# Performance work log

Measured on AMD Instinct MI355X. Metric: run time of the kernel, lower is better.

The kernel has to match this reference:

```python
import jax, jax.numpy as jnp
import numpy as np

TWO_PI = 2.0 * np.pi


def _fftfreq(n, d):
    # numpy-compatible fftfreq, trace/grad-safe in d: [0..n/2-1, -n/2..-1]/(n*d)
    k = jnp.arange(n)
    k = jnp.where(k < (n + 1) // 2, k, k - n).astype(jnp.float32)
    return k / (n * d)


def _forward(x, wp1_re, wp1_im, wp2_re, wp2_im, wr_re, wr_im, ty, tx):
    wp1 = (wp1_re + 1j * wp1_im).astype(jnp.complex64)   # [Ci,Co,m1]
    wp2 = (wp2_re + 1j * wp2_im).astype(jnp.complex64)   # [Ci,Co,m2]
    wr = (wr_re + 1j * wr_im).astype(jnp.complex64)      # [Ci,Co,m1,m2]
    Ny, Nx = x.shape[-2], x.shape[-1]
    dty = ty[1] - ty[0]
    dtx = tx[1] - tx[0]

    alpha = jnp.fft.fft2(x, axes=(-2, -1))               # [B,Ci,Ny,Nx] complex
    lam1 = (1j * TWO_PI * _fftfreq(Ny, dty)).astype(jnp.complex64)  # [Ny]
    lam2 = (1j * TWO_PI * _fftfreq(Nx, dtx)).astype(jnp.complex64)  # [Nx]

    # Pole-residue transfer function factors: Hw = wr / ((lam1-p1)(lam2-p2))
    A1 = 1.0 / (lam1 - wp1[..., None])                   # [Ci,Co,m1,Ny]
    A2 = 1.0 / (lam2 - wp2[..., None])                   # [Ci,Co,m2,Nx]

    # sum over poles (p,q) of Hw -> [Ci,Co,Ny,Nx]
    Hsum = jnp.einsum('ikpq,ikpo,ikqx->ikox', wr, A1, A2)
    res1 = jnp.einsum('biox,ikox->bkox', alpha, Hsum)    # [B,Co,Ny,Nx]
    # sum over frequency grid (o,x) -> residue coefficients [B,Co,m1,m2]
    res2 = jnp.einsum('biox,ikpq,ikpo,ikqx->bkpq', alpha, wr, A1, A2)

    x1 = jnp.real(jnp.fft.ifft2(res1, s=(Ny, Nx), axes=(-2, -1)))

    # explicit pole-exponential evaluation over the spatial grid
    E1 = jnp.exp(wp1[..., None] * ty.astype(jnp.complex64))  # [Ci,Co,m1,Ny]
    E2 = jnp.exp(wp2[..., None] * tx.astype(jnp.complex64))  # [Ci,Co,m2,Nx]
    # res2 channel dim contracts against E1/E2's first (in==out required)
    x2 = jnp.real(jnp.einsum('kbpq,bipz,biqx->kizx', res2, E1, E2)) / (Nx * Ny)
    return x1 + x2


def setup_inputs() -> dict:
    key = jax.random.key(0)
    B, Ci, Co, Ny, Nx, m1, m2 = 8, 32, 32, 128, 128, 4, 5
    ks = jax.random.split(key, 7)
    scale = 1.0 / (Ci * Co)
    x = jax.random.normal(ks[0], (B, Ci, Ny, Nx), jnp.float32)
    wp1_re = scale * jax.random.uniform(ks[1], (Ci, Co, m1), jnp.float32)
    wp1_im = scale * jax.random.uniform(ks[2], (Ci, Co, m1), jnp.float32)
    wp2_re = scale * jax.random.uniform(ks[3], (Ci, Co, m2), jnp.float32)
    wp2_im = scale * jax.random.uniform(ks[4], (Ci, Co, m2), jnp.float32)
    wr_re = scale * jax.random.uniform(ks[5], (Ci, Co, m1, m2), jnp.float32)
    wr_im = scale * jax.random.uniform(ks[6], (Ci, Co, m1, m2), jnp.float32)
    ty = (jnp.arange(Ny) / Ny).astype(jnp.float32)
    tx = (jnp.arange(Nx) / Nx).astype(jnp.float32)
    return dict(x=x, wp1_re=wp1_re, wp1_im=wp1_im, wp2_re=wp2_re, wp2_im=wp2_im,
                wr_re=wr_re, wr_im=wr_im, ty=ty, tx=tx)


def reference(x, wp1_re, wp1_im, wp2_re, wp2_im, wr_re, wr_im, ty, tx):
    return _forward(x, wp1_re, wp1_im, wp2_re, wp2_im, wr_re, wr_im, ty, tx)
```

## Files before the change

kernel.cpp:

```cpp
#include <hip/hip_runtime.h>
#include <math.h>

#define N 128
#define B 8
#define CI 32
#define CO 32
#define M1 4
#define M2 5
#define IK (CI*CO)
#define IKP (IK*M1)
#define IKQ (IK*M2)
#define TWO_PI_F 6.2831853071795864769f

__device__ __forceinline__ float2 cmul(float2 a, float2 b){
    return make_float2(fmaf(a.x,b.x,-(a.y*b.y)), fmaf(a.x,b.y,a.y*b.x));
}
__device__ __forceinline__ float2 cmadd(float2 acc, float2 a, float2 b){
    acc.x = fmaf(a.x, b.x, fmaf(-a.y, b.y, acc.x));
    acc.y = fmaf(a.x, b.y, fmaf( a.y, b.x, acc.y));
    return acc;
}

__global__ void k_A1T(const float* wr_, const float* wi_, const float* t_, float2* A1T){
    int idx = blockIdx.x*256 + threadIdx.x;
    int o   = idx >> 12;
    int ikp = idx & (IKP-1);
    float d = t_[1]-t_[0];
    float invnd = 1.0f/((float)N*d);
    int kk = (o < N/2) ? o : o - N;
    float lam = TWO_PI_F * (float)kk * invnd;
    float dr = -wr_[ikp];
    float di = lam - wi_[ikp];
    float inv = 1.0f/(dr*dr + di*di);
    A1T[idx] = make_float2(dr*inv, -di*inv);
}

__global__ void k_A2(const float* wr_, const float* wi_, const float* t_, float2* A2){
    int idx = blockIdx.x*256 + threadIdx.x;
    int ikq = idx >> 7; int xx = idx & (N-1);
    float d = t_[1]-t_[0];
    float invnd = 1.0f/((float)N*d);
    int kk = (xx < N/2) ? xx : xx - N;
    float lam = TWO_PI_F * (float)kk * invnd;
    float dr = -wr_[ikq];
    float di = lam - wi_[ikq];
    float inv = 1.0f/(dr*dr + di*di);
    A2[idx] = make_float2(dr*inv, -di*inv);
}

__global__ void k_E(const float* wr_, const float* wi_, const float* t_, float2* E){
    int idx = blockIdx.x*256 + threadIdx.x;
    int ikp = idx >> 7; int y = idx & (N-1);
    float t = t_[y];
    float m = expf(wr_[ikp]*t);
    float s, c; sincosf(wi_[ikp]*t, &s, &c);
    E[idx] = make_float2(m*c, m*s);
}

__global__ void k_W2N(const float* wrr, const float* wri, const float2* A2, float2* W2N){
    int idx = blockIdx.x*256 + threadIdx.x;
    int ikp = idx >> 7; int xx = idx & (N-1);
    int ik = ikp >> 2; int p = ikp & 3;
    float2 acc = make_float2(0.f,0.f);
    const float* wr0 = wrr + ik*(M1*M2) + p*M2;
    const float* wi0 = wri + ik*(M1*M2) + p*M2;
    const float2* a2 = A2 + (size_t)ik*(M2*N) + xx;
    #pragma unroll
    for(int q=0;q<M2;q++){
        float2 w = make_float2(wr0[q], wi0[q]);
        acc = cmadd(acc, w, a2[q*N]);
    }
    W2N[(size_t)ikp*N + xx] = acc;
}

template<int SIGNPOS, int REALIN, int SCALE>
__global__ void __launch_bounds__(256) k_fft_rows(const void* in_, float2* out){
    const float sgn = SIGNPOS ? 1.0f : -1.0f;
    __shared__ float tre[16*132];
    __shared__ float tim_[16*132];
    __shared__ float zre[16*136];
    __shared__ float zim[16*136];
    int t = threadIdx.x;
    size_t row0 = (size_t)blockIdx.x * 16;

    if(REALIN){
        const float* src = (const float*)in_ + row0*N;
        #pragma unroll
        for(int j=0;j<8;j++){
            int idx = t + 256*j; int r = idx>>7, cl = idx&127;
            tre[r*132+cl] = src[idx];
        }
    } else {
        const float2* src = (const float2*)in_ + row0*N;
        #pragma unroll
        for(int j=0;j<8;j++){
            int idx = t + 256*j; int r = idx>>7, cl = idx&127;
            float2 v = src[idx];
            tre[r*132+cl] = v.x; tim_[r*132+cl] = v.y;
        }
    }
    float t16c[16], t16s[16];
    #pragma unroll
    for(int j=0;j<16;j++){ float s,c; sincosf(sgn*(TWO_PI_F/16.f)*(float)j, &s,&c); t16c[j]=c; t16s[j]=s; }
    __syncthreads();

    int r = t>>4, u = t&15, b = u&7, h = u>>3;
    float xr[16], xi[16];
    #pragma unroll
    for(int a=0;a<16;a++){
        float vr = tre[r*132 + 8*a + b];
        float vi = REALIN ? 0.f : tim_[r*132 + 8*a + b];
        if(h && (a&1)){ vr = -vr; vi = -vi; }
        xr[a]=vr; xi[a]=vi;
    }
    #pragma unroll
    for(int cc=0; cc<8; cc++){
        float yr=0.f, yi=0.f;
        #pragma unroll
        for(int a=0;a<16;a++){
            int j = (a*cc)&15;
            if(REALIN){
                yr = fmaf(xr[a], t16c[j], yr);
                yi = fmaf(xr[a], t16s[j], yi);
            } else {
                yr = fmaf(xr[a], t16c[j], yr); yr = fmaf(-xi[a], t16s[j], yr);
                yi = fmaf(xr[a], t16s[j], yi); yi = fmaf( xi[a], t16c[j], yi);
            }
        }
        int c = 8*h + cc;
        float s,co; sincosf(sgn*(TWO_PI_F/128.f)*(float)(b*c), &s,&co);
        zre[r*136 + b*17 + c] = fmaf(yr,co,-(yi*s));
        zim[r*136 + b*17 + c] = fmaf(yr,s,  yi*co);
    }
    __syncthreads();

    float t8c[8], t8s[8];
    #pragma unroll
    for(int j=0;j<8;j++){ float s,c; sincosf(sgn*(TWO_PI_F/8.f)*(float)j, &s,&c); t8c[j]=c; t8s[j]=s; }
    int r2 = t>>4, c2 = t&15;
    float zr_[8], zi_[8];
    #pragma unroll
    for(int bb=0;bb<8;bb++){ zr_[bb]=zre[r2*136 + bb*17 + c2]; zi_[bb]=zim[r2*136 + bb*17 + c2]; }
    float2* dst = out + (row0 + r2)*N;
    #pragma unroll
    for(int d=0; d<8; d++){
        float Xr=0.f, Xi=0.f;
        #pragma unroll
        for(int bb=0;bb<8;bb++){
            int j=(bb*d)&7;
            Xr = fmaf(zr_[bb], t8c[j], Xr); Xr = fmaf(-zi_[bb], t8s[j], Xr);
            Xi = fmaf(zr_[bb], t8s[j], Xi); Xi = fmaf( zi_[bb], t8c[j], Xi);
        }
        if(SCALE){ Xr *= (1.f/128.f); Xi *= (1.f/128.f); }
        dst[c2 + 16*d] = make_float2(Xr, Xi);
    }
}

template<int SIGNPOS, int REALOUT, int SCALE>
__global__ void __launch_bounds__(256) k_fft_cols(const float2* in, float2* outc, float* outr){
    const float sgn = SIGNPOS ? 1.0f : -1.0f;
    __shared__ float tre[N*17];
    __shared__ float tim_[N*17];
    __shared__ float zre[8*16*17];
    __shared__ float zim[8*16*17];
    int t = threadIdx.x;
    int img = blockIdx.x >> 3; int x0 = (blockIdx.x & 7)*16;
    const float2* src = in + (size_t)img*N*N + x0;
    #pragma unroll
    for(int j=0;j<8;j++){
        int idx = t + 256*j; int y = idx>>4, xc = idx&15;
        float2 v = src[y*N + xc];
        tre[y*17+xc]=v.x; tim_[y*17+xc]=v.y;
    }
    float t16c[16], t16s[16];
    #pragma unroll
    for(int j=0;j<16;j++){ float s,c; sincosf(sgn*(TWO_PI_F/16.f)*(float)j, &s,&c); t16c[j]=c; t16s[j]=s; }
    __syncthreads();

    int xc = t&15, u = t>>4, b = u&7, h = u>>3;
    float xr[16], xi[16];
    #pragma unroll
    for(int a=0;a<16;a++){
        int y = 8*a + b;
        float vr = tre[y*17+xc];
        float vi = tim_[y*17+xc];
        if(h && (a&1)){ vr = -vr; vi = -vi; }
        xr[a]=vr; xi[a]=vi;
    }
    #pragma unroll
    for(int cc=0; cc<8; cc++){
        float yr=0.f, yi=0.f;
        #pragma unroll
        for(int a=0;a<16;a++){
            int j = (a*cc)&15;
            yr = fmaf(xr[a], t16c[j], yr); yr = fmaf(-xi[a], t16s[j], yr);
            yi = fmaf(xr[a], t16s[j], yi); yi = fmaf( xi[a], t16c[j], yi);
        }
        int c = 8*h + cc;
        float s,co; sincosf(sgn*(TWO_PI_F/128.f)*(float)(b*c), &s,&co);
        zre[(b*16 + c)*17 + xc] = fmaf(yr,co,-(yi*s));
        zim[(b*16 + c)*17 + xc] = fmaf(yr,s,  yi*co);
    }
    __syncthreads();

    float t8c[8], t8s[8];
    #pragma unroll
    for(int j=0;j<8;j++){ float s,c; sincosf(sgn*(TWO_PI_F/8.f)*(float)j, &s,&c); t8c[j]=c; t8s[j]=s; }
    int c2 = t>>4; int x2 = t&15;
    float zr_[8], zi_[8];
    #pragma unroll
    for(int bb=0;bb<8;bb++){ zr_[bb]=zre[(bb*16 + c2)*17 + x2]; zi_[bb]=zim[(bb*16 + c2)*17 + x2]; }
    #pragma unroll
    for(int d=0; d<8; d++){
        float Xr=0.f, Xi=0.f;
        #pragma unroll
        for(int bb=0;bb<8;bb++){
            int j=(bb*d)&7;
            Xr = fmaf(zr_[bb], t8c[j], Xr); Xr = fmaf(-zi_[bb], t8s[j], Xr);
            Xi = fmaf(zr_[bb], t8s[j], Xi); Xi = fmaf( zi_[bb], t8c[j], Xi);
        }
        int ky = c2 + 16*d;
        if(REALOUT){
            outr[(size_t)img*N*N + ky*N + x0 + x2] = Xr * (SCALE ? (1.f/128.f) : 1.f);
        } else {
            if(SCALE){ Xr *= (1.f/128.f); Xi *= (1.f/128.f); }
            outc[(size_t)img*N*N + ky*N + x0 + x2] = make_float2(Xr, Xi);
        }
    }
}

__global__ void __launch_bounds__(256) k_res1(const float2* alpha, const float2* A1T,
                                              const float2* W2N, float2* res1){
    __shared__ float4 At4[B*CI*8];
    int t = threadIdx.x;
    int o  = blockIdx.x >> 3;
    int x0 = (blockIdx.x & 7) * 16;

    {
        int im0 = t >> 3, xq = t & 7;
        #pragma unroll
        for(int j=0;j<8;j++){
            int im = im0 + 32*j;
            At4[im*8 + xq] = *(const float4*)(alpha + (size_t)im*(N*N) + o*N + x0 + 2*xq);
        }
    }
    __syncthreads();

    int k = t >> 3, xh = t & 7;
    float2 acc[B][2];
    #pragma unroll
    for(int b=0;b<B;b++){ acc[b][0]=make_float2(0.f,0.f); acc[b][1]=make_float2(0.f,0.f); }

    const float2* a1base = A1T + (size_t)o*IKP + k*M1;
    const float2* w2base = W2N + ((size_t)k*M1)*N + x0 + 2*xh;

    #pragma unroll 2
    for(int i=0;i<CI;i++){
        float4 a1a = *(const float4*)(a1base + (size_t)i*128);
        float4 a1b = *(const float4*)(a1base + (size_t)i*128 + 2);
        float2 a1v[M1] = { make_float2(a1a.x,a1a.y), make_float2(a1a.z,a1a.w),
                           make_float2(a1b.x,a1b.y), make_float2(a1b.z,a1b.w) };
        float2 h0 = make_float2(0.f,0.f), h1 = make_float2(0.f,0.f);
        const float2* w2 = w2base + (size_t)i*(128*N);
        #pragma unroll
        for(int p=0;p<M1;p++){
            float4 wv = *(const float4*)(w2 + (size_t)p*N);
            h0 = cmadd(h0, a1v[p], make_float2(wv.x,wv.y));
            h1 = cmadd(h1, a1v[p], make_float2(wv.z,wv.w));
        }
        #pragma unroll
        for(int b=0;b<B;b++){
            float4 av = At4[(b*CI + i)*8 + xh];
            acc[b][0] = cmadd(acc[b][0], make_float2(av.x,av.y), h0);
            acc[b][1] = cmadd(acc[b][1], make_float2(av.z,av.w), h1);
        }
    }

    #pragma unroll
    for(int b=0;b<B;b++){
        float4 v = make_float4(acc[b][0].x, acc[b][0].y, acc[b][1].x, acc[b][1].y);
        *(float4*)(res1 + (size_t)(b*CO + k)*(N*N) + o*N + x0 + 2*xh) = v;
    }
}

__global__ void __launch_bounds__(256) k_S_res2(const float2* alpha, const float2* A2,
                                                const float2* A1T, const float* wrr,
                                                const float* wri, float2* res2){
    __shared__ float2 tile[128*17];
    __shared__ float2 A2c[16*40];
    int t = threadIdx.x;
    int ol = t & 31;
    int kl = t >> 5;
    int bid = blockIdx.x;
    int kq = bid & 3;
    int i  = (bid >> 2) & (CI-1);
    int b  = bid >> 7;
    int k0 = kq*8;
    int k  = k0 + kl;
    int ik = i*CO + k;
    const float2* asrc = alpha + ((size_t)(b*CI + i))*(N*N);

    const int trow = t >> 4, txc = t & 15;
    int a2dst[3]; size_t a2src[3]; bool a2ok[3];
    #pragma unroll
    for(int s=0;s<3;s++){
        int e = t + 256*s;
        a2ok[s] = (e < 640);
        int e2 = a2ok[s] ? e : 0;
        int xcs = e2 / 40, rs = e2 - xcs*40;
        int kk = rs / 5, qq = rs - kk*5;
        a2dst[s] = xcs*40 + rs;
        a2src[s] = ((size_t)(i*CO + k0 + kk)*M2 + qq)*N + xcs;
    }

    float2 U[4][5];
    #pragma unroll
    for(int oi=0;oi<4;oi++)
        #pragma unroll
        for(int q=0;q<5;q++) U[oi][q] = make_float2(0.f,0.f);

    float2 pre[8], a2pre[3];
    #pragma unroll
    for(int j=0;j<8;j++) pre[j] = asrc[(trow + 16*j)*N + txc];
    #pragma unroll
    for(int s=0;s<3;s++) if(a2ok[s]) a2pre[s] = A2[a2src[s]];

    for(int c=0; c<8; c++){
        __syncthreads();
        #pragma unroll
        for(int j=0;j<8;j++) tile[(trow + 16*j)*17 + txc] = pre[j];
        #pragma unroll
        for(int s=0;s<3;s++) if(a2ok[s]) A2c[a2dst[s]] = a2pre[s];
        if(c < 7){
            int x0n = (c+1)*16;
            #pragma unroll
            for(int j=0;j<8;j++) pre[j] = asrc[(trow + 16*j)*N + x0n + txc];
            #pragma unroll
            for(int s=0;s<3;s++) if(a2ok[s]) a2pre[s] = A2[a2src[s] + x0n];
        }
        __syncthreads();
        #pragma unroll 4
        for(int xc=0; xc<16; xc++){
            float2 a2v[5];
            const float2* a2row = A2c + xc*40 + kl*5;
            #pragma unroll
            for(int q=0;q<5;q++) a2v[q] = a2row[q];
            #pragma unroll
            for(int oi=0;oi<4;oi++){
                float2 av = tile[(ol + 32*oi)*17 + xc];
                #pragma unroll
                for(int q=0;q<5;q++) U[oi][q] = cmadd(U[oi][q], av, a2v[q]);
            }
        }
    }

    float2 S[4][5];
    #pragma unroll
    for(int p=0;p<4;p++)
        #pragma unroll
        for(int q=0;q<5;q++) S[p][q] = make_float2(0.f,0.f);
    #pragma unroll
    for(int oi=0;oi<4;oi++){
        int o = ol + 32*oi;
        const float2* a1 = A1T + (size_t)o*IKP + (size_t)ik*M1;
        float2 a1v[4];
        #pragma unroll
        for(int p=0;p<4;p++) a1v[p] = a1[p];
        #pragma unroll
        for(int p=0;p<4;p++)
            #pragma unroll
            for(int q=0;q<5;q++) S[p][q] = cmadd(S[p][q], a1v[p], U[oi][q]);
    }
    #pragma unroll
    for(int m=1;m<32;m<<=1){
        #pragma unroll
        for(int p=0;p<4;p++)
            #pragma unroll
            for(int q=0;q<5;q++){
                S[p][q].x += __shfl_xor(S[p][q].x, m);
                S[p][q].y += __shfl_xor(S[p][q].y, m);
            }
    }
    if(ol==0){
        const float* wr0 = wrr + ik*(M1*M2);
        const float* wi0 = wri + ik*(M1*M2);
        float2* dst = res2 + (size_t)(b*CO + k)*(M1*M2);
        #pragma unroll
        for(int p=0;p<4;p++)
            #pragma unroll
            for(int q=0;q<5;q++){
                float2 w = make_float2(wr0[p*5+q], wi0[p*5+q]);
                float2 v = cmul(w, S[p][q]);
                atomicAdd(&dst[p*5+q].x, v.x);
                atomicAdd(&dst[p*5+q].y, v.y);
            }
    }
}

__global__ void __launch_bounds__(256) k_x2(const float2* res2, const float2* E1,
                                            const float2* E2, float* out){
    __shared__ __align__(16) float2 res2s[CI*M1*M2];
    __shared__ __align__(16) float2 Wt[M1*N];
    __shared__ __align__(16) float2 buf[2][M1*64 + M2*N];
    int t = threadIdx.x;
    int yh = blockIdx.x & 1;
    int j  = (blockIdx.x >> 1) & (CO-1);
    int b  = blockIdx.x >> 6;
    int xt = t & 15, yt = t >> 4;

    {
        const float4* s4 = (const float4*)(res2 + (size_t)b*CO*M1*M2);
        float4* d4 = (float4*)res2s;
        d4[t] = s4[t];
        if(t < 64) d4[256+t] = s4[256+t];
    }

    const bool is1_0 = (t < 128);
    const bool ok1 = (t < 192);
    int off0, dst0;
    if(is1_0){ int pp = t >> 5, rem = t & 31; off0 = pp*N + rem*2; dst0 = pp*64 + rem*2; }
    else     { int g = t - 128; int qq = g >> 6, xi = (g & 63) << 1; off0 = qq*N + xi; dst0 = 256 + qq*128 + xi; }
    int qq1 = 2 + (t >> 6), xi1 = (t & 63) << 1;
    int off1 = qq1*N + xi1;
    int dst1 = 256 + qq1*128 + xi1;

    const float2* E1c = E1 + ((size_t)j*M1)*N + yh*64;
    const float2* E2c = E2 + ((size_t)j*M2)*N;

    float4 pre0 = *(const float4*)((is1_0 ? E1c : E2c) + off0);
    float4 pre1 = ok1 ? *(const float4*)(E2c + off1) : make_float4(0.f,0.f,0.f,0.f);
    *(float4*)(&buf[0][dst0]) = pre0;
    if(ok1) *(float4*)(&buf[0][dst1]) = pre1;
    int cur = 0;
    __syncthreads();

    float acc[4][8];
    #pragma unroll
    for(int yy=0;yy<4;yy++)
        #pragma unroll
        for(int s=0;s<8;s++) acc[yy][s] = 0.f;

    for(int c=0; c<CI; c++){
        const float2* E2s = buf[cur] + 256;
        #pragma unroll
        for(int s=0;s<2;s++){
            int e = t + 256*s;
            int pp = e >> 7, xi = e & 127;
            const float2* rr = res2s + c*(M1*M2) + pp*M2;
            float2 w = make_float2(0.f,0.f);
            #pragma unroll
            for(int q=0;q<M2;q++) w = cmadd(w, rr[q], E2s[q*128 + xi]);
            Wt[pp*128 + xi] = w;
        }
        if(c+1 < CI){
            E1c += (size_t)CO*M1*N;
            E2c += (size_t)CO*M2*N;
            pre0 = *(const float4*)((is1_0 ? E1c : E2c) + off0);
            if(ok1) pre1 = *(const float4*)(E2c + off1);
        }
        __syncthreads();

        const float2* E1s = buf[cur];
        float2 e1[4][4];
        #pragma unroll
        for(int p=0;p<4;p++){
            float4 a  = *(const float4*)(E1s + p*64 + yt*4);
            float4 bq = *(const float4*)(E1s + p*64 + yt*4 + 2);
            e1[p][0]=make_float2(a.x,a.y);  e1[p][1]=make_float2(a.z,a.w);
            e1[p][2]=make_float2(bq.x,bq.y); e1[p][3]=make_float2(bq.z,bq.w);
        }
        #pragma unroll
        for(int p=0;p<4;p++){
            #pragma unroll
            for(int s=0;s<4;s++){
                float4 wv = *(const float4*)(Wt + p*128 + 32*s + 2*xt);
                #pragma unroll
                for(int yy=0;yy<4;yy++){
                    float2 e = e1[p][yy];
                    acc[yy][2*s]   = fmaf(e.x, wv.x, fmaf(-e.y, wv.y, acc[yy][2*s]));
                    acc[yy][2*s+1] = fmaf(e.x, wv.z, fmaf(-e.y, wv.w, acc[yy][2*s+1]));
                }
            }
        }
        if(c+1 < CI){
            float2* nb = buf[cur^1];
            *(float4*)(nb + dst0) = pre0;
            if(ok1) *(float4*)(nb + dst1) = pre1;
        }
        cur ^= 1;
        __syncthreads();
    }

    const float sc = 1.0f/((float)N*(float)N);
    size_t base = (size_t)(b*CO + j)*(N*N) + (size_t)yh*64*N;
    #pragma unroll
    for(int yy=0;yy<4;yy++){
        float* orow = out + base + (size_t)(yt*4 + yy)*N;
        #pragma unroll
        for(int s=0;s<4;s++){
            float2* dst = (float2*)(orow + 32*s + 2*xt);
            float2 old = *dst;
            *dst = make_float2(old.x + acc[yy][2*s]*sc, old.y + acc[yy][2*s+1]*sc);
        }
    }
}

extern "C" void kernel_launch(void* const* d_in, const int* in_sizes, int n_in,
                              void* d_out, int out_size, void* d_ws, size_t ws_size,
                              hipStream_t stream){
    const float* x    = (const float*)d_in[0];
    const float* wp1r = (const float*)d_in[1];
    const float* wp1i = (const float*)d_in[2];
    const float* wp2r = (const float*)d_in[3];
    const float* wp2i = (const float*)d_in[4];
    const float* wrr  = (const float*)d_in[5];
    const float* wri  = (const float*)d_in[6];
    const float* ty   = (const float*)d_in[7];
    const float* tx   = (const float*)d_in[8];
    float* out = (float*)d_out;
    float2* ws = (float2*)d_ws;

    const size_t NCIMG = (size_t)B*CI*N*N;
    float2* bufA  = ws;
    float2* alpha = bufA  + NCIMG;
    float2* res1  = alpha + NCIMG;
    float2* A1T   = res1  + NCIMG;
    float2* A2    = A1T   + (size_t)N*IKP;
    float2* W2N   = A2    + (size_t)IKQ*N;
    float2* E1    = W2N   + (size_t)N*IKP;
    float2* E2    = E1    + (size_t)IKP*N;
    float2* res2  = E2    + (size_t)IKQ*N;

    k_A1T<<<(N*IKP)/256, 256, 0, stream>>>(wp1r, wp1i, ty, A1T);
    k_E  <<<(IKP*N)/256, 256, 0, stream>>>(wp1r, wp1i, ty, E1);
    k_A2 <<<(IKQ*N)/256, 256, 0, stream>>>(wp2r, wp2i, tx, A2);
    k_E  <<<(IKQ*N)/256, 256, 0, stream>>>(wp2r, wp2i, tx, E2);
    k_W2N<<<(IKP*N)/256, 256, 0, stream>>>(wrr, wri, A2, W2N);

    k_fft_rows<0,1,0><<<(B*CI*N)/16, 256, 0, stream>>>((const void*)x, bufA);
    k_fft_cols<0,0,0><<<B*CI*8, 256, 0, stream>>>(bufA, alpha, nullptr);

    hipMemsetAsync(res2, 0, (size_t)B*CO*M1*M2*sizeof(float2), stream);
    k_res1<<<N*8, 256, 0, stream>>>(alpha, A1T, W2N, res1);
    k_S_res2<<<B*CI*4, 256, 0, stream>>>(alpha, A2, A1T, wrr, wri, res2);

    k_fft_rows<1,0,1><<<(B*CO*N)/16, 256, 0, stream>>>((const void*)res1, bufA);
    k_fft_cols<1,1,1><<<B*CO*8, 256, 0, stream>>>(bufA, nullptr, out);
    k_x2<<<B*CO*2, 256, 0, stream>>>(res2, E1, E2, out);
}
```

Baseline: 355.2 us.

## Enlarge per-block work tiles in res2 and x2 kernels to reuse loads

```diff
diff --git a/kernel.cpp b/kernel.cpp
--- a/kernel.cpp
+++ b/kernel.cpp
@@ -287,67 +287,65 @@
                                                 const float2* A1T, const float* wrr,
                                                 const float* wri, float2* res2){
     __shared__ float2 tile[128*17];
-    __shared__ float2 A2c[16*40];
+    __shared__ float2 A2c[16*80];
     int t = threadIdx.x;
-    int ol = t & 31;
-    int kl = t >> 5;
+    int ol = t & 15;
+    int kl = t >> 4;
     int bid = blockIdx.x;
-    int kq = bid & 3;
-    int i  = (bid >> 2) & (CI-1);
-    int b  = bid >> 7;
-    int k0 = kq*8;
+    int kh = bid & 1;
+    int i  = (bid >> 1) & (CI-1);
+    int b  = bid >> 6;
+    int k0 = kh*16;
     int k  = k0 + kl;
     int ik = i*CO + k;
     const float2* asrc = alpha + ((size_t)(b*CI + i))*(N*N);
 
     const int trow = t >> 4, txc = t & 15;
-    int a2dst[3]; size_t a2src[3]; bool a2ok[3];
-    #pragma unroll
-    for(int s=0;s<3;s++){
+    int a2dst[5]; size_t a2src[5];
+    #pragma unroll
+    for(int s=0;s<5;s++){
         int e = t + 256*s;
-        a2ok[s] = (e < 640);
-        int e2 = a2ok[s] ? e : 0;
-        int xcs = e2 / 40, rs = e2 - xcs*40;
+        int xcs = e / 80, rs = e - xcs*80;
         int kk = rs / 5, qq = rs - kk*5;
-        a2dst[s] = xcs*40 + rs;
+        a2dst[s] = xcs*80 + rs;
         a2src[s] = ((size_t)(i*CO + k0 + kk)*M2 + qq)*N + xcs;
     }
 
-    float2 U[4][5];
-    #pragma unroll
-    for(int oi=0;oi<4;oi++)
+    float2 U[8][5];
+    #pragma unroll
+    for(int oi=0;oi<8;oi++)
         #pragma unroll
         for(int q=0;q<5;q++) U[oi][q] = make_float2(0.f,0.f);
 
-    float2 pre[8], a2pre[3];
+    float2 pre[8], a2pre[5];
     #pragma unroll
     for(int j=0;j<8;j++) pre[j] = asrc[(trow + 16*j)*N + txc];
     #pragma unroll
-    for(int s=0;s<3;s++) if(a2ok[s]) a2pre[s] = A2[a2src[s]];
+    for(int s=0;s<5;s++) a2pre[s] = A2[a2src[s]];
 
     for(int c=0; c<8; c++){
         __syncthreads();
         #pragma unroll
         for(int j=0;j<8;j++) tile[(trow + 16*j)*17 + txc] = pre[j];
         #pragma unroll
-        for(int s=0;s<3;s++) if(a2ok[s]) A2c[a2dst[s]] = a2pre[s];
+        for(int s=0;s<5;s++) A2c[a2dst[s]] = a2pre[s];
         if(c < 7){
             int x0n = (c+1)*16;
             #pragma unroll
             for(int j=0;j<8;j++) pre[j] = asrc[(trow + 16*j)*N + x0n + txc];
             #pragma unroll
-            for(int s=0;s<3;s++) if(a2ok[s]) a2pre[s] = A2[a2src[s] + x0n];
+            for(int s=0;s<5;s++) a2pre[s] = A2[a2src[s] + x0n];
         }
         __syncthreads();
-        #pragma unroll 4
+        #pragma unroll 2
         for(int xc=0; xc<16; xc++){
             float2 a2v[5];
-            const float2* a2row = A2c + xc*40 + kl*5;
+            const float2* a2row = A2c + xc*80 + kl*5;
             #pragma unroll
             for(int q=0;q<5;q++) a2v[q] = a2row[q];
             #pragma unroll
-            for(int oi=0;oi<4;oi++){
-                float2 av = tile[(ol + 32*oi)*17 + xc];
+            for(int oi=0;oi<8;oi++){
+                float2 av = tile[(ol + 16*oi)*17 + xc];
                 #pragma unroll
                 for(int q=0;q<5;q++) U[oi][q] = cmadd(U[oi][q], av, a2v[q]);
             }
@@ -360,8 +358,8 @@
         #pragma unroll
         for(int q=0;q<5;q++) S[p][q] = make_float2(0.f,0.f);
     #pragma unroll
-    for(int oi=0;oi<4;oi++){
-        int o = ol + 32*oi;
+    for(int oi=0;oi<8;oi++){
+        int o = ol + 16*oi;
         const float2* a1 = A1T + (size_t)o*IKP + (size_t)ik*M1;
         float2 a1v[4];
         #pragma unroll
@@ -372,7 +370,7 @@
             for(int q=0;q<5;q++) S[p][q] = cmadd(S[p][q], a1v[p], U[oi][q]);
     }
     #pragma unroll
-    for(int m=1;m<32;m<<=1){
+    for(int m=1;m<16;m<<=1){
         #pragma unroll
         for(int p=0;p<4;p++)
             #pragma unroll
@@ -401,11 +399,10 @@
                                             const float2* E2, float* out){
     __shared__ __align__(16) float2 res2s[CI*M1*M2];
     __shared__ __align__(16) float2 Wt[M1*N];
-    __shared__ __align__(16) float2 buf[2][M1*64 + M2*N];
+    __shared__ __align__(16) float2 buf[2][M1*N + M2*N];
     int t = threadIdx.x;
-    int yh = blockIdx.x & 1;
-    int j  = (blockIdx.x >> 1) & (CO-1);
-    int b  = blockIdx.x >> 6;
+    int j  = blockIdx.x & (CO-1);
+    int b  = blockIdx.x >> 5;
     int xt = t & 15, yt = t >> 4;
 
     {
@@ -415,33 +412,34 @@
         if(t < 64) d4[256+t] = s4[256+t];
     }
 
-    const bool is1_0 = (t < 128);
-    const bool ok1 = (t < 192);
-    int off0, dst0;
-    if(is1_0){ int pp = t >> 5, rem = t & 31; off0 = pp*N + rem*2; dst0 = pp*64 + rem*2; }
-    else     { int g = t - 128; int qq = g >> 6, xi = (g & 63) << 1; off0 = qq*N + xi; dst0 = 256 + qq*128 + xi; }
-    int qq1 = 2 + (t >> 6), xi1 = (t & 63) << 1;
-    int off1 = qq1*N + xi1;
-    int dst1 = 256 + qq1*128 + xi1;
-
-    const float2* E1c = E1 + ((size_t)j*M1)*N + yh*64;
+    const bool ok2 = (t < 64);
+    int pp0 = t >> 6, rem0 = (t & 63) << 1;
+    int off0 = pp0*N + rem0,          dst0 = pp0*128 + rem0;
+    int qq1 = t >> 6, xi1 = (t & 63) << 1;
+    int off1 = qq1*N + xi1,           dst1 = 512 + qq1*128 + xi1;
+    int xi2 = (t & 63) << 1;
+    int off2 = 4*N + xi2,             dst2 = 512 + 4*128 + xi2;
+
+    const float2* E1c = E1 + ((size_t)j*M1)*N;
     const float2* E2c = E2 + ((size_t)j*M2)*N;
 
-    float4 pre0 = *(const float4*)((is1_0 ? E1c : E2c) + off0);
-    float4 pre1 = ok1 ? *(const float4*)(E2c + off1) : make_float4(0.f,0.f,0.f,0.f);
+    float4 pre0 = *(const float4*)(E1c + off0);
+    float4 pre1 = *(const float4*)(E2c + off1);
+    float4 pre2 = ok2 ? *(const float4*)(E2c + off2) : make_float4(0.f,0.f,0.f,0.f);
     *(float4*)(&buf[0][dst0]) = pre0;
-    if(ok1) *(float4*)(&buf[0][dst1]) = pre1;
+    *(float4*)(&buf[0][dst1]) = pre1;
+    if(ok2) *(float4*)(&buf[0][dst2]) = pre2;
     int cur = 0;
     __syncthreads();
 
-    float acc[4][8];
-    #pragma unroll
-    for(int yy=0;yy<4;yy++)
+    float acc[8][8];
+    #pragma unroll
+    for(int yy=0;yy<8;yy++)
         #pragma unroll
         for(int s=0;s<8;s++) acc[yy][s] = 0.f;
 
     for(int c=0; c<CI; c++){
-        const float2* E2s = buf[cur] + 256;
+        const float2* E2s = buf[cur] + 512;
         #pragma unroll
         for(int s=0;s<2;s++){
             int e = t + 256*s;
@@ -455,28 +453,28 @@
         if(c+1 < CI){
             E1c += (size_t)CO*M1*N;
             E2c += (size_t)CO*M2*N;
-            pre0 = *(const float4*)((is1_0 ? E1c : E2c) + off0);
-            if(ok1) pre1 = *(const float4*)(E2c + off1);
+            pre0 = *(const float4*)(E1c + off0);
+            pre1 = *(const float4*)(E2c + off1);
+            if(ok2) pre2 = *(const float4*)(E2c + off2);
         }
         __syncthreads();
 
         const float2* E1s = buf[cur];
-        float2 e1[4][4];
         #pragma unroll
         for(int p=0;p<4;p++){
-            float4 a  = *(const float4*)(E1s + p*64 + yt*4);
-            float4 bq = *(const float4*)(E1s + p*64 + yt*4 + 2);
-            e1[p][0]=make_float2(a.x,a.y);  e1[p][1]=make_float2(a.z,a.w);
-            e1[p][2]=make_float2(bq.x,bq.y); e1[p][3]=make_float2(bq.z,bq.w);
-        }
-        #pragma unroll
-        for(int p=0;p<4;p++){
+            float2 e1[8];
+            #pragma unroll
+            for(int g=0;g<4;g++){
+                float4 a = *(const float4*)(E1s + p*128 + yt*8 + 2*g);
+                e1[2*g]   = make_float2(a.x,a.y);
+                e1[2*g+1] = make_float2(a.z,a.w);
+            }
             #pragma unroll
             for(int s=0;s<4;s++){
                 float4 wv = *(const float4*)(Wt + p*128 + 32*s + 2*xt);
                 #pragma unroll
-                for(int yy=0;yy<4;yy++){
-                    float2 e = e1[p][yy];
+                for(int yy=0;yy<8;yy++){
+                    float2 e = e1[yy];
                     acc[yy][2*s]   = fmaf(e.x, wv.x, fmaf(-e.y, wv.y, acc[yy][2*s]));
                     acc[yy][2*s+1] = fmaf(e.x, wv.z, fmaf(-e.y, wv.w, acc[yy][2*s+1]));
                 }
@@ -485,17 +483,18 @@
         if(c+1 < CI){
             float2* nb = buf[cur^1];
             *(float4*)(nb + dst0) = pre0;
-            if(ok1) *(float4*)(nb + dst1) = pre1;
+            *(float4*)(nb + dst1) = pre1;
+            if(ok2) *(float4*)(nb + dst2) = pre2;
         }
         cur ^= 1;
         __syncthreads();
     }
 
     const float sc = 1.0f/((float)N*(float)N);
-    size_t base = (size_t)(b*CO + j)*(N*N) + (size_t)yh*64*N;
-    #pragma unroll
-    for(int yy=0;yy<4;yy++){
-        float* orow = out + base + (size_t)(yt*4 + yy)*N;
+    size_t base = (size_t)(b*CO + j)*(N*N);
+    #pragma unroll
+    for(int yy=0;yy<8;yy++){
+        float* orow = out + base + (size_t)(yt*8 + yy)*N;
         #pragma unroll
         for(int s=0;s<4;s++){
             float2* dst = (float2*)(orow + 32*s + 2*xt);
@@ -542,9 +541,9 @@
 
     hipMemsetAsync(res2, 0, (size_t)B*CO*M1*M2*sizeof(float2), stream);
     k_res1<<<N*8, 256, 0, stream>>>(alpha, A1T, W2N, res1);
-    k_S_res2<<<B*CI*4, 256, 0, stream>>>(alpha, A2, A1T, wrr, wri, res2);
+    k_S_res2<<<B*CI*2, 256, 0, stream>>>(alpha, A2, A1T, wrr, wri, res2);
 
     k_fft_rows<1,0,1><<<(B*CO*N)/16, 256, 0, stream>>>((const void*)res1, bufA);
     k_fft_cols<1,1,1><<<B*CO*8, 256, 0, stream>>>(bufA, nullptr, out);
-    k_x2<<<B*CO*2, 256, 0, stream>>>(res2, E1, E2, out);
-}
+    k_x2<<<B*CO, 256, 0, stream>>>(res2, E1, E2, out);
+}
```

Result: faster. 331.2 us (-6.8%).

## Repartition res2 kernel by row quarter and replace atomics with partial-sum reduction

Applied to the files above, without the earlier changes.

```diff
diff --git a/kernel.cpp b/kernel.cpp
--- a/kernel.cpp
+++ b/kernel.cpp
@@ -48,6 +48,19 @@
     A2[idx] = make_float2(dr*inv, -di*inv);
 }
 
+__global__ void k_A2T(const float* wr_, const float* wi_, const float* t_, float2* A2T){
+    int idx = blockIdx.x*256 + threadIdx.x;
+    int x = idx / IKQ; int ikq = idx - x*IKQ;
+    float d = t_[1]-t_[0];
+    float invnd = 1.0f/((float)N*d);
+    int kk = (x < N/2) ? x : x - N;
+    float lam = TWO_PI_F * (float)kk * invnd;
+    float dr = -wr_[ikq];
+    float di = lam - wi_[ikq];
+    float inv = 1.0f/(dr*dr + di*di);
+    A2T[idx] = make_float2(dr*inv, -di*inv);
+}
+
 __global__ void k_E(const float* wr_, const float* wi_, const float* t_, float2* E){
     int idx = blockIdx.x*256 + threadIdx.x;
     int ikp = idx >> 7; int y = idx & (N-1);
@@ -283,117 +296,136 @@
     }
 }
 
-__global__ void __launch_bounds__(256) k_S_res2(const float2* alpha, const float2* A2,
-                                                const float2* A1T, const float* wrr,
-                                                const float* wri, float2* res2){
-    __shared__ float2 tile[128*17];
-    __shared__ float2 A2c[16*40];
+__global__ void __launch_bounds__(512, 8) k_S_res2(const float2* alpha, const float2* A2T,
+                                                   const float2* A1T, float2* part){
+    __shared__ float2 tile[32*9];
+    __shared__ float2 A2c[8*160];
     int t = threadIdx.x;
-    int ol = t & 31;
-    int kl = t >> 5;
+    int ol = t & 15;
+    int kl = t >> 4;
     int bid = blockIdx.x;
-    int kq = bid & 3;
+    int oq = bid & 3;
     int i  = (bid >> 2) & (CI-1);
     int b  = bid >> 7;
-    int k0 = kq*8;
-    int k  = k0 + kl;
-    int ik = i*CO + k;
-    const float2* asrc = alpha + ((size_t)(b*CI + i))*(N*N);
-
-    const int trow = t >> 4, txc = t & 15;
+    int ik = i*CO + kl;
+    const float2* asrc = alpha + ((size_t)(b*CI + i))*(N*N) + (size_t)oq*32*N;
+
+    const int trow = t >> 3, txc = t & 7;
+    const bool tok = (t < 256);
+
     int a2dst[3]; size_t a2src[3]; bool a2ok[3];
     #pragma unroll
     for(int s=0;s<3;s++){
-        int e = t + 256*s;
-        a2ok[s] = (e < 640);
+        int e = t + 512*s;
+        a2ok[s] = (e < 1280);
         int e2 = a2ok[s] ? e : 0;
-        int xcs = e2 / 40, rs = e2 - xcs*40;
-        int kk = rs / 5, qq = rs - kk*5;
-        a2dst[s] = xcs*40 + rs;
-        a2src[s] = ((size_t)(i*CO + k0 + kk)*M2 + qq)*N + xcs;
-    }
-
-    float2 U[4][5];
-    #pragma unroll
-    for(int oi=0;oi<4;oi++)
+        int xcs = e2 / 160, rs = e2 - xcs*160;
+        a2dst[s] = e2;
+        a2src[s] = (size_t)xcs*IKQ + i*(CO*M2) + rs;
+    }
+
+    float2 U[2][5];
+    #pragma unroll
+    for(int oi=0;oi<2;oi++)
         #pragma unroll
         for(int q=0;q<5;q++) U[oi][q] = make_float2(0.f,0.f);
 
-    float2 pre[8], a2pre[3];
-    #pragma unroll
-    for(int j=0;j<8;j++) pre[j] = asrc[(trow + 16*j)*N + txc];
-    #pragma unroll
-    for(int s=0;s<3;s++) if(a2ok[s]) a2pre[s] = A2[a2src[s]];
-
-    for(int c=0; c<8; c++){
+    float2 pre = make_float2(0.f,0.f), a2pre[3];
+    if(tok) pre = asrc[trow*N + txc];
+    #pragma unroll
+    for(int s=0;s<3;s++) if(a2ok[s]) a2pre[s] = A2T[a2src[s]];
+
+    for(int c=0; c<16; c++){
         __syncthreads();
-        #pragma unroll
-        for(int j=0;j<8;j++) tile[(trow + 16*j)*17 + txc] = pre[j];
+        if(tok) tile[trow*9 + txc] = pre;
         #pragma unroll
         for(int s=0;s<3;s++) if(a2ok[s]) A2c[a2dst[s]] = a2pre[s];
-        if(c < 7){
-            int x0n = (c+1)*16;
-            #pragma unroll
-            for(int j=0;j<8;j++) pre[j] = asrc[(trow + 16*j)*N + x0n + txc];
-            #pragma unroll
-            for(int s=0;s<3;s++) if(a2ok[s]) a2pre[s] = A2[a2src[s] + x0n];
+        if(c < 15){
+            if(tok) pre = asrc[trow*N + (c+1)*8 + txc];
+            #pragma unroll
+            for(int s=0;s<3;s++) if(a2ok[s]) a2pre[s] = A2T[a2src[s] + (size_t)(c+1)*8*IKQ];
         }
         __syncthreads();
-        #pragma unroll 4
-        for(int xc=0; xc<16; xc++){
+        #pragma unroll
+        for(int xc=0; xc<8; xc++){
             float2 a2v[5];
-            const float2* a2row = A2c + xc*40 + kl*5;
+            const float2* a2row = A2c + xc*160 + kl*5;
             #pragma unroll
             for(int q=0;q<5;q++) a2v[q] = a2row[q];
             #pragma unroll
-            for(int oi=0;oi<4;oi++){
-                float2 av = tile[(ol + 32*oi)*17 + xc];
+            for(int oi=0;oi<2;oi++){
+                float2 av = tile[(ol + 16*oi)*9 + xc];
                 #pragma unroll
                 for(int q=0;q<5;q++) U[oi][q] = cmadd(U[oi][q], av, a2v[q]);
             }
         }
     }
 
-    float2 S[4][5];
-    #pragma unroll
-    for(int p=0;p<4;p++)
-        #pragma unroll
-        for(int q=0;q<5;q++) S[p][q] = make_float2(0.f,0.f);
-    #pragma unroll
-    for(int oi=0;oi<4;oi++){
-        int o = ol + 32*oi;
-        const float2* a1 = A1T + (size_t)o*IKP + (size_t)ik*M1;
-        float2 a1v[4];
-        #pragma unroll
-        for(int p=0;p<4;p++) a1v[p] = a1[p];
-        #pragma unroll
-        for(int p=0;p<4;p++)
-            #pragma unroll
-            for(int q=0;q<5;q++) S[p][q] = cmadd(S[p][q], a1v[p], U[oi][q]);
+    #pragma unroll
+    for(int ph=0; ph<2; ph++){
+        float2 S[2][5];
+        #pragma unroll
+        for(int pp2=0;pp2<2;pp2++)
+            #pragma unroll
+            for(int q=0;q<5;q++) S[pp2][q] = make_float2(0.f,0.f);
+        #pragma unroll
+        for(int oi=0;oi<2;oi++){
+            int o = oq*32 + ol + 16*oi;
+            const float2* a1 = A1T + (size_t)o*IKP + (size_t)ik*M1 + ph*2;
+            float2 a1v0 = a1[0], a1v1 = a1[1];
+            #pragma unroll
+            for(int q=0;q<5;q++){
+                S[0][q] = cmadd(S[0][q], a1v0, U[oi][q]);
+                S[1][q] = cmadd(S[1][q], a1v1, U[oi][q]);
+            }
+        }
+        #pragma unroll
+        for(int m=1;m<16;m<<=1){
+            #pragma unroll
+            for(int pp2=0;pp2<2;pp2++)
+                #pragma unroll
+                for(int q=0;q<5;q++){
+                    S[pp2][q].x += __shfl_xor(S[pp2][q].x, m);
+                    S[pp2][q].y += __shfl_xor(S[pp2][q].y, m);
+                }
+        }
+        if(ol==0){
+            float2* dst = part + ((size_t)((b*CO + kl)*CI + i)*4 + oq)*(M1*M2) + ph*2*M2;
+            #pragma unroll
+            for(int pp2=0;pp2<2;pp2++)
+                #pragma unroll
+                for(int q=0;q<5;q++) dst[pp2*5+q] = S[pp2][q];
+        }
+    }
+}
+
+__global__ void k_res2_red(const float2* part, const float* wrr, const float* wri, float2* res2){
+    int bk = blockIdx.x;
+    int t = threadIdx.x;
+    int i = t & 31, g = t >> 5;
+    int k = bk & (CO-1);
+    int ikk = i*CO + k;
+    float2 acc[5];
+    #pragma unroll
+    for(int e=0;e<5;e++){
+        int pq = g*5 + e;
+        float2 w = make_float2(wrr[ikk*(M1*M2)+pq], wri[ikk*(M1*M2)+pq]);
+        const float2* pp = part + ((size_t)(bk*CI + i)*4)*(M1*M2) + pq;
+        float2 s0 = pp[0], s1 = pp[M1*M2], s2 = pp[2*M1*M2], s3 = pp[3*M1*M2];
+        float2 s = make_float2(s0.x+s1.x+s2.x+s3.x, s0.y+s1.y+s2.y+s3.y);
+        acc[e] = cmul(w, s);
     }
     #pragma unroll
     for(int m=1;m<32;m<<=1){
         #pragma unroll
-        for(int p=0;p<4;p++)
-            #pragma unroll
-            for(int q=0;q<5;q++){
-                S[p][q].x += __shfl_xor(S[p][q].x, m);
-                S[p][q].y += __shfl_xor(S[p][q].y, m);
-            }
-    }
-    if(ol==0){
-        const float* wr0 = wrr + ik*(M1*M2);
-        const float* wi0 = wri + ik*(M1*M2);
-        float2* dst = res2 + (size_t)(b*CO + k)*(M1*M2);
-        #pragma unroll
-        for(int p=0;p<4;p++)
-            #pragma unroll
-            for(int q=0;q<5;q++){
-                float2 w = make_float2(wr0[p*5+q], wi0[p*5+q]);
-                float2 v = cmul(w, S[p][q]);
-                atomicAdd(&dst[p*5+q].x, v.x);
-                atomicAdd(&dst[p*5+q].y, v.y);
-            }
+        for(int e=0;e<5;e++){
+            acc[e].x += __shfl_xor(acc[e].x, m);
+            acc[e].y += __shfl_xor(acc[e].y, m);
+        }
+    }
+    if(i==0){
+        #pragma unroll
+        for(int e=0;e<5;e++) res2[(size_t)bk*(M1*M2) + g*5 + e] = acc[e];
     }
 }
 
@@ -418,9 +450,9 @@
     const bool is1_0 = (t < 128);
     const bool ok1 = (t < 192);
     int off0, dst0;
-    if(is1_0){ int pp = t >> 5, rem = t & 31; off0 = pp*N + rem*2; dst0 = pp*64 + rem*2; }
+    if(is1_0){ int pp = t >> 5, rem = (t & 31) << 1; off0 = pp*N + rem; dst0 = pp*64 + rem; }
     else     { int g = t - 128; int qq = g >> 6, xi = (g & 63) << 1; off0 = qq*N + xi; dst0 = 256 + qq*128 + xi; }
-    int qq1 = 2 + (t >> 6), xi1 = (t & 63) << 1;
+    int g1 = t + 128; int qq1 = g1 >> 6, xi1 = (g1 & 63) << 1;
     int off1 = qq1*N + xi1;
     int dst1 = 256 + qq1*128 + xi1;
 
@@ -461,22 +493,19 @@
         __syncthreads();
 
         const float2* E1s = buf[cur];
-        float2 e1[4][4];
         #pragma unroll
         for(int p=0;p<4;p++){
+            float2 e1[4];
             float4 a  = *(const float4*)(E1s + p*64 + yt*4);
             float4 bq = *(const float4*)(E1s + p*64 + yt*4 + 2);
-            e1[p][0]=make_float2(a.x,a.y);  e1[p][1]=make_float2(a.z,a.w);
-            e1[p][2]=make_float2(bq.x,bq.y); e1[p][3]=make_float2(bq.z,bq.w);
-        }
-        #pragma unroll
-        for(int p=0;p<4;p++){
+            e1[0]=make_float2(a.x,a.y);  e1[1]=make_float2(a.z,a.w);
+            e1[2]=make_float2(bq.x,bq.y); e1[3]=make_float2(bq.z,bq.w);
             #pragma unroll
             for(int s=0;s<4;s++){
                 float4 wv = *(const float4*)(Wt + p*128 + 32*s + 2*xt);
                 #pragma unroll
                 for(int yy=0;yy<4;yy++){
-                    float2 e = e1[p][yy];
+                    float2 e = e1[yy];
                     acc[yy][2*s]   = fmaf(e.x, wv.x, fmaf(-e.y, wv.y, acc[yy][2*s]));
                     acc[yy][2*s+1] = fmaf(e.x, wv.z, fmaf(-e.y, wv.w, acc[yy][2*s+1]));
                 }
@@ -526,23 +555,26 @@
     float2* res1  = alpha + NCIMG;
     float2* A1T   = res1  + NCIMG;
     float2* A2    = A1T   + (size_t)N*IKP;
-    float2* W2N   = A2    + (size_t)IKQ*N;
+    float2* A2T   = A2    + (size_t)IKQ*N;
+    float2* W2N   = A2T   + (size_t)N*IKQ;
     float2* E1    = W2N   + (size_t)N*IKP;
     float2* E2    = E1    + (size_t)IKP*N;
     float2* res2  = E2    + (size_t)IKQ*N;
+    float2* part  = res2  + (size_t)B*CO*M1*M2;
 
     k_A1T<<<(N*IKP)/256, 256, 0, stream>>>(wp1r, wp1i, ty, A1T);
     k_E  <<<(IKP*N)/256, 256, 0, stream>>>(wp1r, wp1i, ty, E1);
     k_A2 <<<(IKQ*N)/256, 256, 0, stream>>>(wp2r, wp2i, tx, A2);
+    k_A2T<<<(N*IKQ)/256, 256, 0, stream>>>(wp2r, wp2i, tx, A2T);
     k_E  <<<(IKQ*N)/256, 256, 0, stream>>>(wp2r, wp2i, tx, E2);
     k_W2N<<<(IKP*N)/256, 256, 0, stream>>>(wrr, wri, A2, W2N);
 
     k_fft_rows<0,1,0><<<(B*CI*N)/16, 256, 0, stream>>>((const void*)x, bufA);
     k_fft_cols<0,0,0><<<B*CI*8, 256, 0, stream>>>(bufA, alpha, nullptr);
 
-    hipMemsetAsync(res2, 0, (size_t)B*CO*M1*M2*sizeof(float2), stream);
     k_res1<<<N*8, 256, 0, stream>>>(alpha, A1T, W2N, res1);
-    k_S_res2<<<B*CI*4, 256, 0, stream>>>(alpha, A2, A1T, wrr, wri, res2);
+    k_S_res2<<<B*CI*4, 512, 0, stream>>>(alpha, A2T, A1T, part);
+    k_res2_red<<<B*CO, 128, 0, stream>>>(part, wrr, wri, res2);
 
     k_fft_rows<1,0,1><<<(B*CO*N)/16, 256, 0, stream>>>((const void*)res1, bufA);
     k_fft_cols<1,1,1><<<B*CO*8, 256, 0, stream>>>(bufA, nullptr, out);
```

After: 391.7 us. 10.3% more time.
